# Kernel tuning notes

Measured on AMD Instinct MI355X. Metric: run time of the kernel, lower is better.

Reference implementation:

```python
import jax, jax.numpy as jnp
import numpy as np

B = 1048576  # batch of homography systems
PATCH = 128.0  # canonical patch size, typical for deep-homography nets


def setup_inputs() -> dict:
    key = jax.random.key(0)
    k1, k2 = jax.random.split(key)
    base = jnp.array([[0.0, 0.0], [PATCH, 0.0], [PATCH, PATCH], [0.0, PATCH]], dtype=jnp.float32)
    # jittered patch corners -> well-conditioned, nonsingular DLT systems
    corners_A = base[None, :, :] + 4.0 * jax.random.normal(k1, (B, 4, 2), dtype=jnp.float32)
    delta = 8.0 * jax.random.normal(k2, (B, 4, 2), dtype=jnp.float32)
    return {"corners_A": corners_A, "delta": delta}


def reference(corners_A, delta):
    # corners_A, delta: [B, 4, 2]
    corners_B = corners_A + delta
    u, v = corners_A[..., 0], corners_A[..., 1]    # [B, 4]
    up, vp = corners_B[..., 0], corners_B[..., 1]  # [B, 4]
    z = jnp.zeros_like(u)
    o = jnp.ones_like(u)
    # even rows (2i):   [0, 0, 0, -u, -v, -1,  vp*u,  vp*v],  b = -vp
    # odd rows  (2i+1): [u, v, 1,  0,  0,  0, -up*u, -up*v],  b =  up
    rows_even = jnp.stack([z, z, z, -u, -v, -o, vp * u, vp * v], axis=-1)  # [B, 4, 8]
    rows_odd = jnp.stack([u, v, o, z, z, z, -up * u, -up * v], axis=-1)    # [B, 4, 8]
    Bsz = corners_A.shape[0]
    A = jnp.stack([rows_even, rows_odd], axis=2).reshape(Bsz, 8, 8)  # interleave even/odd rows
    b = jnp.stack([-vp, up], axis=2).reshape(Bsz, 8, 1)
    # square 8x8 system: lstsq solution == linear solve for nonsingular A
    hhat = jnp.linalg.solve(A, b)[..., 0]  # [B, 8]
    H = jnp.concatenate([hhat, jnp.ones((Bsz, 1), dtype=hhat.dtype)], axis=-1).reshape(Bsz, 3, 3)
    return H
```

## Files before the change

### kernel.cpp

```cpp
#include <hip/hip_runtime.h>

#define THREADS 256
#define WAVES 4
#define SPT 2
#define SEG 64
#define SYS_PER_BLOCK (THREADS * SPT)
#define SEG_FLOATS (SEG * 9)
#define SEG_VEC4 (SEG_FLOATS / 4)
#define BLOCK_VEC4 (SYS_PER_BLOCK * 9 / 4)

typedef float vfloat4 __attribute__((ext_vector_type(4)));

__device__ __forceinline__ void solve_h(const vfloat4 c0, const vfloat4 c1,
                                        const vfloat4 e0, const vfloat4 e1,
                                        float h[9])
{
    const float u1 = c0.x, v1 = c0.y, u2 = c0.z, v2 = c0.w;
    const float u3 = c1.x, v3 = c1.y, u4 = c1.z, v4 = c1.w;
    const float p1 = u1 + e0.x, q1 = v1 + e0.y;
    const float p2 = u2 + e0.z, q2 = v2 + e0.w;
    const float p3 = u3 + e1.x, q3 = v3 + e1.y;
    const float p4 = u4 + e1.z, q4 = v4 + e1.w;

    #define DET3(ax,ay,bx,by,cx,cy) \
        (((bx) - (ax)) * ((cy) - (ay)) - ((cx) - (ax)) * ((by) - (ay)))

    const float D1a = DET3(u4, v4, u2, v2, u3, v3);
    const float D2a = DET3(u1, v1, u4, v4, u3, v3);
    const float D3a = DET3(u1, v1, u2, v2, u4, v4);
    const float D1b = DET3(p4, q4, p2, q2, p3, q3);
    const float D2b = DET3(p1, q1, p4, q4, p3, q3);
    const float D3b = DET3(p1, q1, p2, q2, p4, q4);

    const float k1 = D1b * (D2a * D3a);
    const float k2 = D2b * (D3a * D1a);
    const float k3 = D3b * (D1a * D2a);

    const float g1x = v2 - v3, g1y = u3 - u2, g1z = u2 * v3 - u3 * v2;
    const float g2x = v3 - v1, g2y = u1 - u3, g2z = u3 * v1 - u1 * v3;
    const float g3x = v1 - v2, g3y = u2 - u1, g3z = u1 * v2 - u2 * v1;

    const float w1 = k1 * p1, w2 = k2 * p2, w3 = k3 * p3;
    const float x1 = k1 * q1, x2 = k2 * q2, x3 = k3 * q3;

    const float H22 = k1 * g1z + k2 * g2z + k3 * g3z;
    const float r = 1.0f / H22;

    h[0] = (w1 * g1x + w2 * g2x + w3 * g3x) * r;
    h[1] = (w1 * g1y + w2 * g2y + w3 * g3y) * r;
    h[2] = (w1 * g1z + w2 * g2z + w3 * g3z) * r;
    h[3] = (x1 * g1x + x2 * g2x + x3 * g3x) * r;
    h[4] = (x1 * g1y + x2 * g2y + x3 * g3y) * r;
    h[5] = (x1 * g1z + x2 * g2z + x3 * g3z) * r;
    h[6] = (k1 * g1x + k2 * g2x + k3 * g3x) * r;
    h[7] = (k1 * g1y + k2 * g2y + k3 * g3y) * r;
    h[8] = 1.0f;
}

__global__ __launch_bounds__(THREADS) void dlt_kernel(
    const vfloat4* __restrict__ cA,
    const vfloat4* __restrict__ dl,
    vfloat4* __restrict__ out4,
    float* __restrict__ out,
    int B)
{
    __shared__ float lds[WAVES][SPT][SEG_FLOATS];
    const int tid  = threadIdx.x;
    const int lane = tid & 63;
    const int wave = tid >> 6;
    const int blockSysBase = blockIdx.x * SYS_PER_BLOCK;
    const int waveSysBase = blockSysBase + wave * (SPT * SEG);

    if (waveSysBase + SPT * SEG <= B) {
        const int g0 = waveSysBase + lane;
        const int g1 = g0 + SEG;

        const vfloat4 a00 = __builtin_nontemporal_load(&cA[2 * g0 + 0]);
        const vfloat4 a01 = __builtin_nontemporal_load(&cA[2 * g0 + 1]);
        const vfloat4 d00 = __builtin_nontemporal_load(&dl[2 * g0 + 0]);
        const vfloat4 d01 = __builtin_nontemporal_load(&dl[2 * g0 + 1]);
        const vfloat4 a10 = __builtin_nontemporal_load(&cA[2 * g1 + 0]);
        const vfloat4 a11 = __builtin_nontemporal_load(&cA[2 * g1 + 1]);
        const vfloat4 d10 = __builtin_nontemporal_load(&dl[2 * g1 + 0]);
        const vfloat4 d11 = __builtin_nontemporal_load(&dl[2 * g1 + 1]);

        #pragma unroll
        for (int s = 0; s < SPT; ++s) {
            float h[9];
            if (s == 0) solve_h(a00, a01, d00, d01, h);
            else        solve_h(a10, a11, d10, d11, h);

            float* buf = &lds[wave][s][0];
            #pragma unroll
            for (int k = 0; k < 9; ++k) buf[lane * 9 + k] = h[k];

            const vfloat4* buf4 = (const vfloat4*)buf;
            const int segBase4 = (waveSysBase + s * SEG) * 9 / 4;
            __builtin_nontemporal_store(buf4[lane],      &out4[segBase4 + lane]);
            __builtin_nontemporal_store(buf4[lane + 64], &out4[segBase4 + lane + 64]);
            if (lane < SEG_VEC4 - 128)
                __builtin_nontemporal_store(buf4[lane + 128], &out4[segBase4 + lane + 128]);
        }
    } else {
        #pragma unroll
        for (int s = 0; s < SPT; ++s) {
            const int b = waveSysBase + s * SEG + lane;
            if (b < B) {
                const vfloat4 c0 = cA[2 * b + 0];
                const vfloat4 c1 = cA[2 * b + 1];
                const vfloat4 e0 = dl[2 * b + 0];
                const vfloat4 e1 = dl[2 * b + 1];
                float h[9];
                solve_h(c0, c1, e0, e1, h);
                #pragma unroll
                for (int k = 0; k < 9; ++k) out[b * 9 + k] = h[k];
            }
        }
    }
}

extern "C" void kernel_launch(void* const* d_in, const int* in_sizes, int n_in,
                              void* d_out, int out_size, void* d_ws, size_t ws_size,
                              hipStream_t stream) {
    const int B = in_sizes[0] / 8;
    const vfloat4* cA = (const vfloat4*)d_in[0];
    const vfloat4* dl = (const vfloat4*)d_in[1];
    vfloat4* out4 = (vfloat4*)d_out;
    float* out = (float*)d_out;
    const int grid = (B + SYS_PER_BLOCK - 1) / SYS_PER_BLOCK;
    dlt_kernel<<<grid, THREADS, 0, stream>>>(cA, dl, out4, out, B);
}
```

Before: 23.98 us.

## Coalesce input loads with lane shuffles and stage block output through shared memory

Each thread now handles one system instead of two. Input is loaded as contiguous float4s across the wave, and each lane's two corner vectors are reassembled with xor-1 lane shuffles, so the per-lane stride-2 access pattern goes away. Results are staged for the whole block in LDS behind a __syncthreads and written out as block-wide float4 nontemporal stores. The cost is twice as many blocks, a block-level barrier, shuffle instructions, and plain instead of nontemporal input loads.

```diff
diff --git a/kernel.cpp b/kernel.cpp
--- a/kernel.cpp
+++ b/kernel.cpp
@@ -1,15 +1,20 @@
 #include <hip/hip_runtime.h>
 
 #define THREADS 256
-#define WAVES 4
-#define SPT 2
-#define SEG 64
-#define SYS_PER_BLOCK (THREADS * SPT)
-#define SEG_FLOATS (SEG * 9)
-#define SEG_VEC4 (SEG_FLOATS / 4)
-#define BLOCK_VEC4 (SYS_PER_BLOCK * 9 / 4)
+#define WAVE_SYS 64
+#define BLOCK_FLOATS (THREADS * 9)
+#define BLOCK_VEC4 (BLOCK_FLOATS / 4)
 
 typedef float vfloat4 __attribute__((ext_vector_type(4)));
+
+__device__ __forceinline__ vfloat4 shflx1_v4(vfloat4 v) {
+    vfloat4 r;
+    r.x = __shfl_xor(v.x, 1, 64);
+    r.y = __shfl_xor(v.y, 1, 64);
+    r.z = __shfl_xor(v.z, 1, 64);
+    r.w = __shfl_xor(v.w, 1, 64);
+    return r;
+}
 
 __device__ __forceinline__ void solve_h(const vfloat4 c0, const vfloat4 c1,
                                         const vfloat4 e0, const vfloat4 e1,
@@ -58,63 +63,73 @@
 }
 
 __global__ __launch_bounds__(THREADS) void dlt_kernel(
-    const vfloat4* __restrict__ cA,
-    const vfloat4* __restrict__ dl,
+    const vfloat4* __restrict__ cA4,
+    const vfloat4* __restrict__ dl4,
     vfloat4* __restrict__ out4,
     float* __restrict__ out,
     int B)
 {
-    __shared__ float lds[WAVES][SPT][SEG_FLOATS];
+    __shared__ float lds[BLOCK_FLOATS];
     const int tid  = threadIdx.x;
     const int lane = tid & 63;
     const int wave = tid >> 6;
-    const int blockSysBase = blockIdx.x * SYS_PER_BLOCK;
-    const int waveSysBase = blockSysBase + wave * (SPT * SEG);
+    const int blockSysBase = blockIdx.x * THREADS;
+    const int waveSysBase  = blockSysBase + wave * WAVE_SYS;
+    const bool odd = (lane & 1) != 0;
+    const int sysLocal = (lane >> 1) + (odd ? 32 : 0);
 
-    if (waveSysBase + SPT * SEG <= B) {
-        const int g0 = waveSysBase + lane;
-        const int g1 = g0 + SEG;
+    const bool fullWave = (waveSysBase + WAVE_SYS) <= B;
+    float h[9];
+    #pragma unroll
+    for (int k = 0; k < 9; ++k) h[k] = 0.0f;
 
-        const vfloat4 a00 = __builtin_nontemporal_load(&cA[2 * g0 + 0]);
-        const vfloat4 a01 = __builtin_nontemporal_load(&cA[2 * g0 + 1]);
-        const vfloat4 d00 = __builtin_nontemporal_load(&dl[2 * g0 + 0]);
-        const vfloat4 d01 = __builtin_nontemporal_load(&dl[2 * g0 + 1]);
-        const vfloat4 a10 = __builtin_nontemporal_load(&cA[2 * g1 + 0]);
-        const vfloat4 a11 = __builtin_nontemporal_load(&cA[2 * g1 + 1]);
-        const vfloat4 d10 = __builtin_nontemporal_load(&dl[2 * g1 + 0]);
-        const vfloat4 d11 = __builtin_nontemporal_load(&dl[2 * g1 + 1]);
+    if (fullWave) {
+        const int vb = 2 * waveSysBase;
+        const vfloat4 rA0 = cA4[vb + lane];
+        const vfloat4 rA1 = cA4[vb + 64 + lane];
+        const vfloat4 rD0 = dl4[vb + lane];
+        const vfloat4 rD1 = dl4[vb + 64 + lane];
 
+        const vfloat4 tA = shflx1_v4(odd ? rA0 : rA1);
+        const vfloat4 tD = shflx1_v4(odd ? rD0 : rD1);
+
+        const vfloat4 c0 = odd ? tA : rA0;
+        const vfloat4 c1 = odd ? rA1 : tA;
+        const vfloat4 e0 = odd ? tD : rD0;
+        const vfloat4 e1 = odd ? rD1 : tD;
+
+        solve_h(c0, c1, e0, e1, h);
+    } else {
+        const int b = waveSysBase + sysLocal;
+        if (b < B) {
+            const vfloat4 c0 = cA4[2 * b + 0];
+            const vfloat4 c1 = cA4[2 * b + 1];
+            const vfloat4 e0 = dl4[2 * b + 0];
+            const vfloat4 e1 = dl4[2 * b + 1];
+            solve_h(c0, c1, e0, e1, h);
+        }
+    }
+
+    float* buf = &lds[wave * (WAVE_SYS * 9)];
+    #pragma unroll
+    for (int k = 0; k < 9; ++k) buf[sysLocal * 9 + k] = h[k];
+    __syncthreads();
+
+    if ((blockSysBase + THREADS) <= B) {
+        const vfloat4* l4 = (const vfloat4*)lds;
+        const int base4 = blockIdx.x * BLOCK_VEC4;
         #pragma unroll
-        for (int s = 0; s < SPT; ++s) {
-            float h[9];
-            if (s == 0) solve_h(a00, a01, d00, d01, h);
-            else        solve_h(a10, a11, d10, d11, h);
-
-            float* buf = &lds[wave][s][0];
-            #pragma unroll
-            for (int k = 0; k < 9; ++k) buf[lane * 9 + k] = h[k];
-
-            const vfloat4* buf4 = (const vfloat4*)buf;
-            const int segBase4 = (waveSysBase + s * SEG) * 9 / 4;
-            __builtin_nontemporal_store(buf4[lane],      &out4[segBase4 + lane]);
-            __builtin_nontemporal_store(buf4[lane + 64], &out4[segBase4 + lane + 64]);
-            if (lane < SEG_VEC4 - 128)
-                __builtin_nontemporal_store(buf4[lane + 128], &out4[segBase4 + lane + 128]);
+        for (int k = 0; k < 3; ++k) {
+            const int i = k * THREADS + tid;
+            if (i < BLOCK_VEC4)
+                __builtin_nontemporal_store(l4[i], &out4[base4 + i]);
         }
     } else {
-        #pragma unroll
-        for (int s = 0; s < SPT; ++s) {
-            const int b = waveSysBase + s * SEG + lane;
-            if (b < B) {
-                const vfloat4 c0 = cA[2 * b + 0];
-                const vfloat4 c1 = cA[2 * b + 1];
-                const vfloat4 e0 = dl[2 * b + 0];
-                const vfloat4 e1 = dl[2 * b + 1];
-                float h[9];
-                solve_h(c0, c1, e0, e1, h);
-                #pragma unroll
-                for (int k = 0; k < 9; ++k) out[b * 9 + k] = h[k];
-            }
+        const int baseF = blockSysBase * 9;
+        const int totalF = B * 9;
+        for (int i = tid; i < BLOCK_FLOATS; i += THREADS) {
+            const int gi = baseF + i;
+            if (gi < totalF) out[gi] = lds[i];
         }
     }
 }
@@ -123,10 +138,10 @@
                               void* d_out, int out_size, void* d_ws, size_t ws_size,
                               hipStream_t stream) {
     const int B = in_sizes[0] / 8;
-    const vfloat4* cA = (const vfloat4*)d_in[0];
-    const vfloat4* dl = (const vfloat4*)d_in[1];
+    const vfloat4* cA4 = (const vfloat4*)d_in[0];
+    const vfloat4* dl4 = (const vfloat4*)d_in[1];
     vfloat4* out4 = (vfloat4*)d_out;
     float* out = (float*)d_out;
-    const int grid = (B + SYS_PER_BLOCK - 1) / SYS_PER_BLOCK;
-    dlt_kernel<<<grid, THREADS, 0, stream>>>(cA, dl, out4, out, B);
+    const int grid = (B + THREADS - 1) / THREADS;
+    dlt_kernel<<<grid, THREADS, 0, stream>>>(cA4, dl4, out4, out, B);
 }
```

Result: faster. 20.77 us (-13.4%).
